# Kernel tuning notes

Hardware: AMD Instinct MI355X
Metric: run time of the kernel (lower is better)

The kernel has to match this reference:

```python
import jax, jax.numpy as jnp
import numpy as np

NUM_HEADS = 8
D_MODEL = 512
HEAD_DIM = D_MODEL // NUM_HEADS
LN_EPS = 1e-5


def setup_inputs() -> dict:
    key = jax.random.key(0)
    ks = jax.random.split(key, 12)
    B, S = 8, 1024
    P = 2 * S - 1  # relative position length
    s = 0.02
    return {
        "x": jax.random.normal(ks[0], (B, S, D_MODEL), jnp.float32),
        "pos_emb": jax.random.normal(ks[1], (P, D_MODEL), jnp.float32),
        "ln_w": jnp.ones((D_MODEL,), jnp.float32),
        "ln_b": jnp.zeros((D_MODEL,), jnp.float32),
        "Wq": jax.random.normal(ks[2], (D_MODEL, D_MODEL), jnp.float32) * s,
        "bq": jax.random.normal(ks[3], (D_MODEL,), jnp.float32) * s,
        "Wk": jax.random.normal(ks[4], (D_MODEL, D_MODEL), jnp.float32) * s,
        "bk": jax.random.normal(ks[5], (D_MODEL,), jnp.float32) * s,
        "Wv": jax.random.normal(ks[6], (D_MODEL, D_MODEL), jnp.float32) * s,
        "bv": jax.random.normal(ks[7], (D_MODEL,), jnp.float32) * s,
        "Wo": jax.random.normal(ks[8], (D_MODEL, D_MODEL), jnp.float32) * s,
        "bo": jax.random.normal(ks[9], (D_MODEL,), jnp.float32) * s,
        "Wp": jax.random.normal(ks[10], (D_MODEL, D_MODEL), jnp.float32) * s,
        "pos_bias_u": jax.random.normal(ks[11], (D_MODEL,), jnp.float32) * s,
        "pos_bias_v": jax.random.normal(jax.random.fold_in(key, 99), (D_MODEL,), jnp.float32) * s,
    }


def _rel_shift(x):
    # x: [B, H, S, P] -> Transformer-XL relative shift, return [B, H, S, S]
    b, h, s, p = x.shape
    x = jnp.pad(x, ((0, 0), (0, 0), (0, 0), (1, 0)))  # pad one zero column on left
    x = x.reshape(b, h, p + 1, s)[:, :, 1:, :]
    x = x.reshape(b, h, s, p)
    return x[:, :, :, :s]


def reference(x, pos_emb, ln_w, ln_b, Wq, bq, Wk, bk, Wv, bv, Wo, bo, Wp,
              pos_bias_u, pos_bias_v):
    B, S, D = x.shape
    H, hd = NUM_HEADS, HEAD_DIM
    # LayerNorm
    mu = jnp.mean(x, axis=-1, keepdims=True)
    var = jnp.mean(jnp.square(x - mu), axis=-1, keepdims=True)
    h_ = (x - mu) * jax.lax.rsqrt(var + LN_EPS) * ln_w + ln_b
    # Projections (torch Linear: y = x @ W.T + b)
    q = (h_ @ Wq.T + bq).reshape(B, S, H, hd).transpose(0, 2, 1, 3)  # [B,H,S,hd]
    k = (h_ @ Wk.T + bk).reshape(B, S, H, hd).transpose(0, 2, 1, 3)
    v = (h_ @ Wv.T + bv).reshape(B, S, H, hd).transpose(0, 2, 1, 3)
    bias_u = pos_bias_u.reshape(1, H, 1, hd)
    bias_v = pos_bias_v.reshape(1, H, 1, hd)
    content = jnp.einsum('bhqd,bhkd->bhqk', q + bias_u, k)
    # Positional projection: [P, D] -> [H, P, hd]
    p = (pos_emb @ Wp.T).reshape(-1, H, hd).transpose(1, 0, 2)
    pos_score = jnp.einsum('bhqd,hpd->bhqp', q + bias_v, p)
    pos_score = _rel_shift(pos_score)
    scale = 1.0 / np.sqrt(hd).astype(np.float32)
    attn = jax.nn.softmax((content + pos_score) * scale, axis=-1)
    out = jnp.einsum('bhqk,bhkd->bhqd', attn, v)
    out = out.transpose(0, 2, 1, 3).reshape(B, S, D)
    out = out @ Wo.T + bo
    return x + out
```

## Files before the change

kernel.cpp:

```cpp
#include <hip/hip_runtime.h>
#include <hip/hip_bf16.h>


typedef __attribute__((ext_vector_type(8))) short  s16x8;
typedef __attribute__((ext_vector_type(8))) __bf16 bfv8;
typedef __attribute__((ext_vector_type(4))) float  f32x4;
typedef __attribute__((ext_vector_type(4))) unsigned u32x4;

__device__ __forceinline__ float b2f(short s){
  unsigned u = ((unsigned)(unsigned short)s) << 16;
  float f; __builtin_memcpy(&f, &u, 4); return f;
}
__device__ __forceinline__ short f2b(float f){
  unsigned u; __builtin_memcpy(&u, &f, 4);
  u = (u + 0x7fffu + ((u >> 16) & 1u)) >> 16;
  return (short)u;
}
__device__ __forceinline__ unsigned pk2(float lo, float hi){
  __hip_bfloat162 t = __float22bfloat162_rn(make_float2(lo, hi));
  unsigned u; __builtin_memcpy(&u, &t, 4); return u;
}
__device__ __forceinline__ f32x4 MFMA(s16x8 a, s16x8 b, f32x4 c){
  return __builtin_amdgcn_mfma_f32_16x16x32_bf16(
      __builtin_bit_cast(bfv8, a), __builtin_bit_cast(bfv8, b), c, 0, 0, 0);
}
__device__ __forceinline__ void gload_lds16(const void* g, void* l){
  __builtin_amdgcn_global_load_lds(
      (const __attribute__((address_space(1))) void*)g,
      (__attribute__((address_space(3))) void*)l, 16, 0, 0);
}
__device__ __forceinline__ void cvt8(const float* in, short* out, size_t i8){
  f32x4 a = *(const f32x4*)(in + i8*8);
  f32x4 b = *(const f32x4*)(in + i8*8 + 4);
  u32x4 o;
  o[0] = pk2(a[0],a[1]); o[1] = pk2(a[2],a[3]);
  o[2] = pk2(b[0],b[1]); o[3] = pk2(b[2],b[3]);
  *(u32x4*)(out + i8*8) = o;
}

__global__ __launch_bounds__(256) void prep_kernel(
    const float* __restrict__ Wq, const float* __restrict__ Wk,
    const float* __restrict__ Wv, const float* __restrict__ Wo,
    const float* __restrict__ Wp, const float* __restrict__ pos,
    const float* __restrict__ x, const float* __restrict__ lnw, const float* __restrict__ lnb,
    short* __restrict__ wqkv, short* __restrict__ wo, short* __restrict__ wp,
    short* __restrict__ posbf, short* __restrict__ h_bf)
{
  int bid = blockIdx.x, tid = threadIdx.x;
  if(bid < 640){
    int w = bid >> 7;
    size_t i = (size_t)(bid & 127)*256 + tid;
    const float* src; short* dst;
    if(w == 0){ src = Wq; dst = wqkv; }
    else if(w == 1){ src = Wk; dst = wqkv + 262144; }
    else if(w == 2){ src = Wv; dst = wqkv + 524288; }
    else if(w == 3){ src = Wo; dst = wo; }
    else { src = Wp; dst = wp; }
    cvt8(src, dst, i);
  } else if(bid < 1152){
    size_t i = (size_t)(bid - 640)*256 + tid;
    if(i < 131008) cvt8(pos, posbf, i);
  } else {
    int row = (bid - 1152)*4 + (tid >> 6);
    int lane = tid & 63;
    const float* xr = x + (size_t)row*512;
    f32x4 v0 = *(const f32x4*)(xr + lane*8);
    f32x4 v1 = *(const f32x4*)(xr + lane*8 + 4);
    float s  = v0[0]+v0[1]+v0[2]+v0[3]+v1[0]+v1[1]+v1[2]+v1[3];
    float s2 = v0[0]*v0[0]+v0[1]*v0[1]+v0[2]*v0[2]+v0[3]*v0[3]
             + v1[0]*v1[0]+v1[1]*v1[1]+v1[2]*v1[2]+v1[3]*v1[3];
    #pragma unroll
    for(int m=1;m<64;m<<=1){ s += __shfl_xor(s,m); s2 += __shfl_xor(s2,m); }
    float mu = s * (1.0f/512.0f);
    float rs = rsqrtf(s2*(1.0f/512.0f) - mu*mu + 1e-5f);
    float y[8];
    #pragma unroll
    for(int e=0;e<8;e++){
      float xv = (e<4)? v0[e] : v1[e-4];
      int d = lane*8 + e;
      y[e] = (xv - mu)*rs*lnw[d] + lnb[d];
    }
    u32x4 o;
    o[0]=pk2(y[0],y[1]); o[1]=pk2(y[2],y[3]); o[2]=pk2(y[4],y[5]); o[3]=pk2(y[6],y[7]);
    *(u32x4*)(h_bf + (size_t)row*512 + lane*8) = o;
  }
}

__global__ __launch_bounds__(256) void gemm_fused(
    const short* __restrict__ h_bf, const short* __restrict__ wqkv,
    const float* __restrict__ bq, const float* __restrict__ bk, const float* __restrict__ bv,
    const short* __restrict__ posbf, const short* __restrict__ wp,
    short* __restrict__ q_sw, short* __restrict__ k_sw, short* __restrict__ v_sw,
    short* __restrict__ p_sw)
{
  __shared__ __align__(16) short smem[9216];
  short* At = smem;
  short* Bt = smem + 4096;
  int bid = blockIdx.x, tid = threadIdx.x;
  int wave = tid >> 6, lane = tid & 63;
  int quad = lane >> 4, l16 = lane & 15;
  int srow = lane >> 2, scol = (lane & 3)*8;
  if(bid < 768){
    int bx = bid % 12, by = bid / 12;
    int m0 = by*128, n0 = bx*128;
    int wm = wave >> 1, wn = wave & 1;
    f32x4 acc[4][4] = {};
    for(int k0=0; k0<512; k0+=32){
      #pragma unroll
      for(int c=0;c<2;c++){
        int rb = (wave + 4*c)*16;
        gload_lds16(h_bf + (size_t)(m0 + rb + srow)*512 + k0 + scol, At + rb*32);
        gload_lds16(wqkv + (size_t)(n0 + rb + srow)*512 + k0 + scol, Bt + rb*32);
      }
      __syncthreads();
      s16x8 af[4], bfr[4];
      #pragma unroll
      for(int i=0;i<4;i++) af[i]  = *(const s16x8*)(At + (wm*64 + i*16 + l16)*32 + quad*8);
      #pragma unroll
      for(int j=0;j<4;j++) bfr[j] = *(const s16x8*)(Bt + (wn*64 + j*16 + l16)*32 + quad*8);
      #pragma unroll
      for(int i=0;i<4;i++)
        #pragma unroll
        for(int j=0;j<4;j++)
          acc[i][j] = MFMA(af[i], bfr[j], acc[i][j]);
      __syncthreads();
    }
    int seg = bx >> 2;
    int nseg = (bx & 3)*128;
    int bb = by >> 3;
    const float* bsrc = (seg==0)? bq : (seg==1)? bk : bv;
    float bias_j[4];
    #pragma unroll
    for(int j=0;j<4;j++) bias_j[j] = bsrc[nseg + wn*64 + j*16 + l16];
    if(seg < 2){
      short* dst = seg ? k_sw : q_sw;
      #pragma unroll
      for(int h2=0; h2<2; h2++){
        if(wm == h2){
          #pragma unroll
          for(int i=0;i<4;i++){
            int lr = i*16 + quad*4;
            #pragma unroll
            for(int j=0;j<4;j++){
              int cl = wn*64 + j*16 + l16;
              unsigned p01 = pk2(acc[i][j][0]+bias_j[j], acc[i][j][1]+bias_j[j]);
              unsigned p23 = pk2(acc[i][j][2]+bias_j[j], acc[i][j][3]+bias_j[j]);
              smem[(lr+0)*136 + cl] = (short)p01;
              smem[(lr+1)*136 + cl] = (short)(p01>>16);
              smem[(lr+2)*136 + cl] = (short)p23;
              smem[(lr+3)*136 + cl] = (short)(p23>>16);
            }
          }
        }
        __syncthreads();
        #pragma unroll
        for(int it=0; it<4; it++){
          int ci = it*4 + wave;
          int hs = ci >> 2, tb = ci & 3;
          s16x8 vv = *(const s16x8*)(smem + (tb*16 + l16)*136 + hs*32 + quad*8);
          int hh = (nseg>>6) + (hs>>1);
          int tg = ((m0 + h2*64)>>4) + tb;
          size_t chunk = ((size_t)((bb*8 + hh)*64 + tg))*2 + (hs&1);
          *(s16x8*)(dst + chunk*512 + (size_t)lane*8) = vv;
        }
        __syncthreads();
      }
    } else {
      #pragma unroll
      for(int h2=0; h2<2; h2++){
        int jt = by*2 + h2;
        if(wm == h2){
          #pragma unroll
          for(int i=0;i<4;i++){
            int tl = i*16 + quad*4;
            #pragma unroll
            for(int j=0;j<4;j++){
              int dl = wn*64 + j*16 + l16;
              unsigned p01 = pk2(acc[i][j][0]+bias_j[j], acc[i][j][1]+bias_j[j]);
              unsigned p23 = pk2(acc[i][j][2]+bias_j[j], acc[i][j][3]+bias_j[j]);
              unsigned* w2 = (unsigned*)(smem + dl*72 + tl);
              w2[0] = p01; w2[1] = p23;
            }
          }
        }
        __syncthreads();
        #pragma unroll
        for(int it=0; it<4; it++){
          int ci = it*4 + wave;
          int hl = ci>>3, ds = (ci>>1)&3, jk = ci&1;
          s16x8 vv = *(const s16x8*)(smem + (hl*64 + ds*16 + l16)*72 + jk*32 + quad*8);
          int hh = (nseg>>6) + hl;
          size_t chunk = (((size_t)((bb*8 + hh)*16 + jt))*4 + ds)*2 + jk;
          *(s16x8*)(v_sw + chunk*512 + (size_t)lane*8) = vv;
        }
        __syncthreads();
      }
    }
  } else {
    int pid = bid - 768;
    int bx = pid % 8, by = pid / 8;
    int m0 = by*64, n0 = bx*64;
    int wm = wave >> 1, wn = wave & 1;
    f32x4 acc[2][2] = {};
    for(int k0=0; k0<512; k0+=32){
      int rb = wave*16;
      int ra = m0 + rb + srow; if(ra > 2046) ra = 2046;
      gload_lds16(posbf + (size_t)ra*512 + k0 + scol, At + rb*32);
      gload_lds16(wp + (size_t)(n0 + rb + srow)*512 + k0 + scol, Bt + rb*32);
      __syncthreads();
      s16x8 af[2], bfr[2];
      #pragma unroll
      for(int i=0;i<2;i++) af[i]  = *(const s16x8*)(At + (wm*32 + i*16 + l16)*32 + quad*8);
      #pragma unroll
      for(int j=0;j<2;j++) bfr[j] = *(const s16x8*)(Bt + (wn*32 + j*16 + l16)*32 + quad*8);
      #pragma unroll
      for(int i=0;i<2;i++)
        #pragma unroll
        for(int j=0;j<2;j++)
          acc[i][j] = MFMA(af[i], bfr[j], acc[i][j]);
      __syncthreads();
    }
    #pragma unroll
    for(int i=0;i<2;i++){
      int rowb = m0 + wm*32 + i*16 + quad*4;
      #pragma unroll
      for(int j=0;j<2;j++){
        int col = n0 + wn*32 + j*16 + l16;
        int hh = col>>6, ks = (col>>5)&1, qd = (col>>3)&3, e = col&7;
        int rblk = rowb>>4;
        size_t base = ((size_t)(((hh*128+rblk)*2+ks)*64) + qd*16)*8 + e;
        #pragma unroll
        for(int r=0;r<4;r++)
          p_sw[base + (size_t)(quad*4+r)*8] = f2b(acc[i][j][r]);
      }
    }
  }
}

__global__ __launch_bounds__(256) void attn_kernel(
    const short* __restrict__ q_sw, const short* __restrict__ k_sw,
    const short* __restrict__ v_sw, const short* __restrict__ p_sw,
    const float* __restrict__ bu, const float* __restrict__ bvv,
    short* __restrict__ out)
{
  __shared__ __align__(16) float combf[4160];
  int tid = threadIdx.x;
  int wave = tid >> 6, lane = tid & 63, quad = lane >> 4, l16 = lane & 15;
  int h = blockIdx.y, b = blockIdx.z, bh = b*8 + h;
  int iblk = blockIdx.x;
  int iw = iblk*16;
  short* pw = (short*)combf + wave*1152;

  const short* qb = q_sw + (size_t)bh*65536;
  const short* kb = k_sw + (size_t)bh*65536;
  const short* vb = v_sw + (size_t)bh*65536;
  const short* pb = p_sw + (size_t)h*131072;

  s16x8 qu[2], qv[2];
  #pragma unroll
  for(int ks=0;ks<2;ks++){
    s16x8 qr = *(const s16x8*)(qb + ((size_t)(iblk*2+ks)*64 + lane)*8);
    short tu[8], tv[8];
    #pragma unroll
    for(int e=0;e<8;e++){
      int d = h*64 + ks*32 + quad*8 + e;
      float f = b2f(qr[e]);
      tu[e] = f2b((f + bu[d]) * 0.125f);
      tv[e] = f2b((f + bvv[d]) * 0.125f);
    }
    qu[ks] = *(s16x8*)tu; qv[ks] = *(s16x8*)tv;
  }

  s16x8 ones;
  #pragma unroll
  for(int e=0;e<8;e++) ones[e] = (short)0x3F80;

  int srcl[4]; bool lo[4];
  #pragma unroll
  for(int r=0;r<4;r++){
    int il = quad*4 + r;
    srcl[r] = quad*16 + ((l16 + 15 - il) & 15);
    lo[r]   = (l16 <= il);
  }

  f32x4 oacc[4] = {};
  f32x4 lacc = {};

  #pragma unroll
  for(int t=0; t<4; t++){
    int jt = wave*4 + t;
    int rb0 = (jt*64 - iw + 1008) >> 4;
    f32x4 ps[5];
    #pragma unroll
    for(int nt=0;nt<5;nt++){
      f32x4 a = {};
      #pragma unroll
      for(int ks=0;ks<2;ks++){
        s16x8 pf = *(const s16x8*)(pb + ((size_t)((rb0+nt)*2+ks)*64 + lane)*8);
        a = MFMA(qv[ks], pf, a);
      }
      ps[nt] = a;
    }
    float rot[4][5];
    #pragma unroll
    for(int r=0;r<4;r++)
      #pragma unroll
      for(int nt=0;nt<5;nt++) rot[r][nt] = __shfl(ps[nt][r], srcl[r]);
    float pe[4][4];
    #pragma unroll
    for(int js=0;js<4;js++){
      f32x4 c0;
      #pragma unroll
      for(int r=0;r<4;r++) c0[r] = lo[r] ? rot[r][js] : rot[r][js+1];
      f32x4 a = c0;
      #pragma unroll
      for(int ks=0;ks<2;ks++){
        s16x8 kf = *(const s16x8*)(kb + ((size_t)((jt*4+js)*2+ks)*64 + lane)*8);
        a = MFMA(qu[ks], kf, a);
      }
      #pragma unroll
      for(int r=0;r<4;r++) pe[js][r] = __expf(a[r]);
    }
    #pragma unroll
    for(int js=0;js<4;js++){
      int col = js*16 + l16;
      unsigned p01 = pk2(pe[js][0], pe[js][1]);
      unsigned p23 = pk2(pe[js][2], pe[js][3]);
      pw[(quad*4+0)*72 + col] = (short)p01;
      pw[(quad*4+1)*72 + col] = (short)(p01>>16);
      pw[(quad*4+2)*72 + col] = (short)p23;
      pw[(quad*4+3)*72 + col] = (short)(p23>>16);
    }
    #pragma unroll
    for(int jk=0;jk<2;jk++){
      s16x8 pf = *(const s16x8*)(pw + l16*72 + jk*32 + quad*8);
      #pragma unroll
      for(int ds=0;ds<4;ds++){
        s16x8 vf = *(const s16x8*)(vb + ((size_t)((jt*4+ds)*2+jk)*64 + lane)*8);
        oacc[ds] = MFMA(pf, vf, oacc[ds]);
      }
      lacc = MFMA(pf, ones, lacc);
    }
  }
  __syncthreads();
  float* comb  = combf;
  float* lcomb = combf + 4096;
  #pragma unroll
  for(int e=0;e<16;e++) comb[wave*1024 + e*64 + lane] = oacc[e>>2][e&3];
  if(l16 == 0){
    #pragma unroll
    for(int r=0;r<4;r++) lcomb[wave*16 + quad*4 + r] = lacc[r];
  }
  __syncthreads();
  #pragma unroll
  for(int i=0;i<4;i++){
    int s = i*256 + tid;
    int e = s >> 6, lsrc = s & 63;
    int ds = e >> 2, rr = e & 3;
    int il = (lsrc >> 4)*4 + rr;
    int dim = ds*16 + (lsrc & 15);
    float o = comb[s] + comb[1024+s] + comb[2048+s] + comb[3072+s];
    float l = lcomb[il] + lcomb[16+il] + lcomb[32+il] + lcomb[48+il];
    float rl = __builtin_amdgcn_rcpf(l);
    out[((size_t)(b*1024 + iw + il)*512) + h*64 + dim] = f2b(o * rl);
  }
}

__global__ __launch_bounds__(256) void gemm_out(
    const short* __restrict__ A, const short* __restrict__ B,
    const float* __restrict__ bias, const float* __restrict__ resid,
    float* __restrict__ Cout)
{
  __shared__ __align__(16) short At[64*32];
  __shared__ __align__(16) short Bt[64*32];
  int tid = threadIdx.x;
  int wave = tid >> 6, lane = tid & 63;
  int quad = lane >> 4, l16 = lane & 15;
  int wm = wave >> 1, wn = wave & 1;
  int m0 = blockIdx.y*64, n0 = blockIdx.x*64;
  int srow = lane >> 2, scol = (lane & 3)*8;
  f32x4 acc[2][2] = {};
  for(int k0=0; k0<512; k0+=32){
    int rb = wave*16;
    gload_lds16(A + (size_t)(m0 + rb + srow)*512 + k0 + scol, At + rb*32);
    gload_lds16(B + (size_t)(n0 + rb + srow)*512 + k0 + scol, Bt + rb*32);
    __syncthreads();
    s16x8 af[2], bfr[2];
    #pragma unroll
    for(int i=0;i<2;i++) af[i]  = *(const s16x8*)(At + (wm*32 + i*16 + l16)*32 + quad*8);
    #pragma unroll
    for(int j=0;j<2;j++) bfr[j] = *(const s16x8*)(Bt + (wn*32 + j*16 + l16)*32 + quad*8);
    #pragma unroll
    for(int i=0;i<2;i++)
      #pragma unroll
      for(int j=0;j<2;j++)
        acc[i][j] = MFMA(af[i], bfr[j], acc[i][j]);
    __syncthreads();
  }
  #pragma unroll
  for(int i=0;i<2;i++){
    int rowb = m0 + wm*32 + i*16 + quad*4;
    #pragma unroll
    for(int j=0;j<2;j++){
      int col = n0 + wn*32 + j*16 + l16;
      float bv = bias[col];
      #pragma unroll
      for(int r=0;r<4;r++){
        size_t idx = (size_t)(rowb + r)*512 + col;
        Cout[idx] = acc[i][j][r] + bv + resid[idx];
      }
    }
  }
}

extern "C" void kernel_launch(void* const* d_in, const int* in_sizes, int n_in,
                              void* d_out, int out_size, void* d_ws, size_t ws_size,
                              hipStream_t stream)
{
  const float* x    = (const float*)d_in[0];
  const float* pos  = (const float*)d_in[1];
  const float* lnw  = (const float*)d_in[2];
  const float* lnb  = (const float*)d_in[3];
  const float* Wq   = (const float*)d_in[4];
  const float* bq   = (const float*)d_in[5];
  const float* Wk   = (const float*)d_in[6];
  const float* bk   = (const float*)d_in[7];
  const float* Wv   = (const float*)d_in[8];
  const float* bv   = (const float*)d_in[9];
  const float* Wo   = (const float*)d_in[10];
  const float* bo   = (const float*)d_in[11];
  const float* Wp   = (const float*)d_in[12];
  const float* pbu  = (const float*)d_in[13];
  const float* pbv  = (const float*)d_in[14];
  float* out = (float*)d_out;

  char* ws = (char*)d_ws;
  short* h_bf    = (short*)(ws);
  short* q_sw    = (short*)(ws + ( 8u<<20));
  short* k_sw    = (short*)(ws + (16u<<20));
  short* v_sw    = (short*)(ws + (24u<<20));
  short* a_bf    = (short*)(ws + (32u<<20));
  short* p_sw    = (short*)(ws + (40u<<20));
  short* pos_bf  = (short*)(ws + (42u<<20));
  short* wqkv_bf = (short*)(ws + (44u<<20));
  short* wo_bf   = (short*)(ws + (47u<<20));
  short* wp_bf   = (short*)(ws + (47u<<20) + (512u<<10));

  prep_kernel<<<dim3(3200), 256, 0, stream>>>(Wq, Wk, Wv, Wo, Wp, pos,
                                              x, lnw, lnb,
                                              wqkv_bf, wo_bf, wp_bf, pos_bf, h_bf);
  gemm_fused<<<dim3(1024), 256, 0, stream>>>(h_bf, wqkv_bf, bq, bk, bv,
                                             pos_bf, wp_bf,
                                             q_sw, k_sw, v_sw, p_sw);
  attn_kernel<<<dim3(64,8,8), 256, 0, stream>>>(q_sw, k_sw, v_sw, p_sw, pbu, pbv, a_bf);
  gemm_out<<<dim3(8,128), 256, 0, stream>>>(a_bf, wo_bf, bo, x, out);
  (void)in_sizes; (void)n_in; (void)out_size; (void)ws_size;
}
```

Measured before the change: 209.5 us.

## Deepen GEMM K-tiles to 64 and give each attention wave its own query rows

Result: slower. 247.5 us (+18.1%).

```diff
diff --git a/kernel.cpp b/kernel.cpp
--- a/kernel.cpp
+++ b/kernel.cpp
@@ -16,6 +16,9 @@
   u = (u + 0x7fffu + ((u >> 16) & 1u)) >> 16;
   return (short)u;
 }
+__device__ __forceinline__ unsigned pk2r(float lo, float hi){
+  return (unsigned)(unsigned short)f2b(lo) | ((unsigned)(unsigned short)f2b(hi) << 16);
+}
 __device__ __forceinline__ unsigned pk2(float lo, float hi){
   __hip_bfloat162 t = __float22bfloat162_rn(make_float2(lo, hi));
   unsigned u; __builtin_memcpy(&u, &t, 4); return u;
@@ -33,8 +36,8 @@
   f32x4 a = *(const f32x4*)(in + i8*8);
   f32x4 b = *(const f32x4*)(in + i8*8 + 4);
   u32x4 o;
-  o[0] = pk2(a[0],a[1]); o[1] = pk2(a[2],a[3]);
-  o[2] = pk2(b[0],b[1]); o[3] = pk2(b[2],b[3]);
+  o[0] = pk2r(a[0],a[1]); o[1] = pk2r(a[2],a[3]);
+  o[2] = pk2r(b[0],b[1]); o[3] = pk2r(b[2],b[3]);
   *(u32x4*)(out + i8*8) = o;
 }
 
@@ -81,7 +84,7 @@
       y[e] = (xv - mu)*rs*lnw[d] + lnb[d];
     }
     u32x4 o;
-    o[0]=pk2(y[0],y[1]); o[1]=pk2(y[2],y[3]); o[2]=pk2(y[4],y[5]); o[3]=pk2(y[6],y[7]);
+    o[0]=pk2r(y[0],y[1]); o[1]=pk2r(y[2],y[3]); o[2]=pk2r(y[4],y[5]); o[3]=pk2r(y[6],y[7]);
     *(u32x4*)(h_bf + (size_t)row*512 + lane*8) = o;
   }
 }
@@ -93,36 +96,39 @@
     short* __restrict__ q_sw, short* __restrict__ k_sw, short* __restrict__ v_sw,
     short* __restrict__ p_sw)
 {
-  __shared__ __align__(16) short smem[9216];
+  __shared__ __align__(16) short smem[16384];
   short* At = smem;
-  short* Bt = smem + 4096;
+  short* Bt = smem + 8192;
   int bid = blockIdx.x, tid = threadIdx.x;
   int wave = tid >> 6, lane = tid & 63;
   int quad = lane >> 4, l16 = lane & 15;
-  int srow = lane >> 2, scol = (lane & 3)*8;
   if(bid < 768){
     int bx = bid % 12, by = bid / 12;
     int m0 = by*128, n0 = bx*128;
     int wm = wave >> 1, wn = wave & 1;
+    int sr8 = lane >> 3, sc = (lane & 7)*8;
     f32x4 acc[4][4] = {};
-    for(int k0=0; k0<512; k0+=32){
-      #pragma unroll
-      for(int c=0;c<2;c++){
-        int rb = (wave + 4*c)*16;
-        gload_lds16(h_bf + (size_t)(m0 + rb + srow)*512 + k0 + scol, At + rb*32);
-        gload_lds16(wqkv + (size_t)(n0 + rb + srow)*512 + k0 + scol, Bt + rb*32);
+    for(int k0=0; k0<512; k0+=64){
+      #pragma unroll
+      for(int c=0;c<4;c++){
+        int ci = wave*4 + c;
+        gload_lds16(h_bf + (size_t)(m0 + ci*8 + sr8)*512 + k0 + sc, At + ci*512);
+        gload_lds16(wqkv + (size_t)(n0 + ci*8 + sr8)*512 + k0 + sc, Bt + ci*512);
       }
       __syncthreads();
-      s16x8 af[4], bfr[4];
-      #pragma unroll
-      for(int i=0;i<4;i++) af[i]  = *(const s16x8*)(At + (wm*64 + i*16 + l16)*32 + quad*8);
-      #pragma unroll
-      for(int j=0;j<4;j++) bfr[j] = *(const s16x8*)(Bt + (wn*64 + j*16 + l16)*32 + quad*8);
-      #pragma unroll
-      for(int i=0;i<4;i++)
-        #pragma unroll
-        for(int j=0;j<4;j++)
-          acc[i][j] = MFMA(af[i], bfr[j], acc[i][j]);
+      #pragma unroll
+      for(int ks2=0;ks2<2;ks2++){
+        s16x8 af[4], bfr[4];
+        #pragma unroll
+        for(int i=0;i<4;i++) af[i]  = *(const s16x8*)(At + (wm*64 + i*16 + l16)*64 + ks2*32 + quad*8);
+        #pragma unroll
+        for(int j=0;j<4;j++) bfr[j] = *(const s16x8*)(Bt + (wn*64 + j*16 + l16)*64 + ks2*32 + quad*8);
+        #pragma unroll
+        for(int i=0;i<4;i++)
+          #pragma unroll
+          for(int j=0;j<4;j++)
+            acc[i][j] = MFMA(af[i], bfr[j], acc[i][j]);
+      }
       __syncthreads();
     }
     int seg = bx >> 2;
@@ -143,8 +149,8 @@
             #pragma unroll
             for(int j=0;j<4;j++){
               int cl = wn*64 + j*16 + l16;
-              unsigned p01 = pk2(acc[i][j][0]+bias_j[j], acc[i][j][1]+bias_j[j]);
-              unsigned p23 = pk2(acc[i][j][2]+bias_j[j], acc[i][j][3]+bias_j[j]);
+              unsigned p01 = pk2r(acc[i][j][0]+bias_j[j], acc[i][j][1]+bias_j[j]);
+              unsigned p23 = pk2r(acc[i][j][2]+bias_j[j], acc[i][j][3]+bias_j[j]);
               smem[(lr+0)*136 + cl] = (short)p01;
               smem[(lr+1)*136 + cl] = (short)(p01>>16);
               smem[(lr+2)*136 + cl] = (short)p23;
@@ -176,8 +182,8 @@
             #pragma unroll
             for(int j=0;j<4;j++){
               int dl = wn*64 + j*16 + l16;
-              unsigned p01 = pk2(acc[i][j][0]+bias_j[j], acc[i][j][1]+bias_j[j]);
-              unsigned p23 = pk2(acc[i][j][2]+bias_j[j], acc[i][j][3]+bias_j[j]);
+              unsigned p01 = pk2r(acc[i][j][0]+bias_j[j], acc[i][j][1]+bias_j[j]);
+              unsigned p23 = pk2r(acc[i][j][2]+bias_j[j], acc[i][j][3]+bias_j[j]);
               unsigned* w2 = (unsigned*)(smem + dl*72 + tl);
               w2[0] = p01; w2[1] = p23;
             }
@@ -197,22 +203,24 @@
       }
     }
   } else {
+    short* Bt2 = smem + 2048;
     int pid = bid - 768;
     int bx = pid % 8, by = pid / 8;
     int m0 = by*64, n0 = bx*64;
     int wm = wave >> 1, wn = wave & 1;
+    int srow = lane >> 2, scol = (lane & 3)*8;
     f32x4 acc[2][2] = {};
     for(int k0=0; k0<512; k0+=32){
       int rb = wave*16;
       int ra = m0 + rb + srow; if(ra > 2046) ra = 2046;
       gload_lds16(posbf + (size_t)ra*512 + k0 + scol, At + rb*32);
-      gload_lds16(wp + (size_t)(n0 + rb + srow)*512 + k0 + scol, Bt + rb*32);
+      gload_lds16(wp + (size_t)(n0 + rb + srow)*512 + k0 + scol, Bt2 + rb*32);
       __syncthreads();
       s16x8 af[2], bfr[2];
       #pragma unroll
       for(int i=0;i<2;i++) af[i]  = *(const s16x8*)(At + (wm*32 + i*16 + l16)*32 + quad*8);
       #pragma unroll
-      for(int j=0;j<2;j++) bfr[j] = *(const s16x8*)(Bt + (wn*32 + j*16 + l16)*32 + quad*8);
+      for(int j=0;j<2;j++) bfr[j] = *(const s16x8*)(Bt2 + (wn*32 + j*16 + l16)*32 + quad*8);
       #pragma unroll
       for(int i=0;i<2;i++)
         #pragma unroll
@@ -243,13 +251,13 @@
     const float* __restrict__ bu, const float* __restrict__ bvv,
     short* __restrict__ out)
 {
-  __shared__ __align__(16) float combf[4160];
+  __shared__ __align__(16) short pwall[4*1152];
   int tid = threadIdx.x;
   int wave = tid >> 6, lane = tid & 63, quad = lane >> 4, l16 = lane & 15;
   int h = blockIdx.y, b = blockIdx.z, bh = b*8 + h;
-  int iblk = blockIdx.x;
-  int iw = iblk*16;
-  short* pw = (short*)combf + wave*1152;
+  int iw = blockIdx.x*64 + wave*16;
+  int tblk = blockIdx.x*4 + wave;
+  short* pw = pwall + wave*1152;
 
   const short* qb = q_sw + (size_t)bh*65536;
   const short* kb = k_sw + (size_t)bh*65536;
@@ -259,7 +267,7 @@
   s16x8 qu[2], qv[2];
   #pragma unroll
   for(int ks=0;ks<2;ks++){
-    s16x8 qr = *(const s16x8*)(qb + ((size_t)(iblk*2+ks)*64 + lane)*8);
+    s16x8 qr = *(const s16x8*)(qb + ((size_t)(tblk*2+ks)*64 + lane)*8);
     short tu[8], tv[8];
     #pragma unroll
     for(int e=0;e<8;e++){
@@ -286,9 +294,8 @@
   f32x4 oacc[4] = {};
   f32x4 lacc = {};
 
-  #pragma unroll
-  for(int t=0; t<4; t++){
-    int jt = wave*4 + t;
+  #pragma unroll 2
+  for(int jt=0; jt<16; jt++){
     int rb0 = (jt*64 - iw + 1008) >> 4;
     f32x4 ps[5];
     #pragma unroll
@@ -309,10 +316,9 @@
     float pe[4][4];
     #pragma unroll
     for(int js=0;js<4;js++){
-      f32x4 c0;
-      #pragma unroll
-      for(int r=0;r<4;r++) c0[r] = lo[r] ? rot[r][js] : rot[r][js+1];
-      f32x4 a = c0;
+      f32x4 a;
+      #pragma unroll
+      for(int r=0;r<4;r++) a[r] = lo[r] ? rot[r][js] : rot[r][js+1];
       #pragma unroll
       for(int ks=0;ks<2;ks++){
         s16x8 kf = *(const s16x8*)(kb + ((size_t)((jt*4+js)*2+ks)*64 + lane)*8);
@@ -342,27 +348,16 @@
       lacc = MFMA(pf, ones, lacc);
     }
   }
-  __syncthreads();
-  float* comb  = combf;
-  float* lcomb = combf + 4096;
-  #pragma unroll
-  for(int e=0;e<16;e++) comb[wave*1024 + e*64 + lane] = oacc[e>>2][e&3];
-  if(l16 == 0){
-    #pragma unroll
-    for(int r=0;r<4;r++) lcomb[wave*16 + quad*4 + r] = lacc[r];
-  }
-  __syncthreads();
-  #pragma unroll
-  for(int i=0;i<4;i++){
-    int s = i*256 + tid;
-    int e = s >> 6, lsrc = s & 63;
-    int ds = e >> 2, rr = e & 3;
-    int il = (lsrc >> 4)*4 + rr;
-    int dim = ds*16 + (lsrc & 15);
-    float o = comb[s] + comb[1024+s] + comb[2048+s] + comb[3072+s];
-    float l = lcomb[il] + lcomb[16+il] + lcomb[32+il] + lcomb[48+il];
-    float rl = __builtin_amdgcn_rcpf(l);
-    out[((size_t)(b*1024 + iw + il)*512) + h*64 + dim] = f2b(o * rl);
+  float rl[4];
+  #pragma unroll
+  for(int r=0;r<4;r++) rl[r] = 1.0f / lacc[r];
+  #pragma unroll
+  for(int ds=0; ds<4; ds++){
+    #pragma unroll
+    for(int r=0;r<4;r++){
+      int row = iw + quad*4 + r;
+      out[((size_t)(b*1024 + row)*512) + h*64 + ds*16 + l16] = f2b(oacc[ds][r] * rl[r]);
+    }
   }
 }
 
@@ -371,30 +366,36 @@
     const float* __restrict__ bias, const float* __restrict__ resid,
     float* __restrict__ Cout)
 {
-  __shared__ __align__(16) short At[64*32];
-  __shared__ __align__(16) short Bt[64*32];
+  __shared__ __align__(16) short At[64*64];
+  __shared__ __align__(16) short Bt[64*64];
   int tid = threadIdx.x;
   int wave = tid >> 6, lane = tid & 63;
   int quad = lane >> 4, l16 = lane & 15;
   int wm = wave >> 1, wn = wave & 1;
   int m0 = blockIdx.y*64, n0 = blockIdx.x*64;
-  int srow = lane >> 2, scol = (lane & 3)*8;
+  int sr8 = lane >> 3, sc = (lane & 7)*8;
   f32x4 acc[2][2] = {};
-  for(int k0=0; k0<512; k0+=32){
-    int rb = wave*16;
-    gload_lds16(A + (size_t)(m0 + rb + srow)*512 + k0 + scol, At + rb*32);
-    gload_lds16(B + (size_t)(n0 + rb + srow)*512 + k0 + scol, Bt + rb*32);
+  for(int k0=0; k0<512; k0+=64){
+    #pragma unroll
+    for(int c=0;c<2;c++){
+      int ci = wave*2 + c;
+      gload_lds16(A + (size_t)(m0 + ci*8 + sr8)*512 + k0 + sc, At + ci*512);
+      gload_lds16(B + (size_t)(n0 + ci*8 + sr8)*512 + k0 + sc, Bt + ci*512);
+    }
     __syncthreads();
-    s16x8 af[2], bfr[2];
-    #pragma unroll
-    for(int i=0;i<2;i++) af[i]  = *(const s16x8*)(At + (wm*32 + i*16 + l16)*32 + quad*8);
-    #pragma unroll
-    for(int j=0;j<2;j++) bfr[j] = *(const s16x8*)(Bt + (wn*32 + j*16 + l16)*32 + quad*8);
-    #pragma unroll
-    for(int i=0;i<2;i++)
-      #pragma unroll
-      for(int j=0;j<2;j++)
-        acc[i][j] = MFMA(af[i], bfr[j], acc[i][j]);
+    #pragma unroll
+    for(int ks2=0;ks2<2;ks2++){
+      s16x8 af[2], bfr[2];
+      #pragma unroll
+      for(int i=0;i<2;i++) af[i]  = *(const s16x8*)(At + (wm*32 + i*16 + l16)*64 + ks2*32 + quad*8);
+      #pragma unroll
+      for(int j=0;j<2;j++) bfr[j] = *(const s16x8*)(Bt + (wn*32 + j*16 + l16)*64 + ks2*32 + quad*8);
+      #pragma unroll
+      for(int i=0;i<2;i++)
+        #pragma unroll
+        for(int j=0;j<2;j++)
+          acc[i][j] = MFMA(af[i], bfr[j], acc[i][j]);
+    }
     __syncthreads();
   }
   #pragma unroll
@@ -452,7 +453,7 @@
   gemm_fused<<<dim3(1024), 256, 0, stream>>>(h_bf, wqkv_bf, bq, bk, bv,
                                              pos_bf, wp_bf,
                                              q_sw, k_sw, v_sw, p_sw);
-  attn_kernel<<<dim3(64,8,8), 256, 0, stream>>>(q_sw, k_sw, v_sw, p_sw, pbu, pbv, a_bf);
+  attn_kernel<<<dim3(16,8,8), 256, 0, stream>>>(q_sw, k_sw, v_sw, p_sw, pbu, pbv, a_bf);
   gemm_out<<<dim3(8,128), 256, 0, stream>>>(a_bf, wo_bf, bo, x, out);
   (void)in_sizes; (void)n_in; (void)out_size; (void)ws_size;
 }
```
